# Performance work log

Measured on AMD Instinct MI355X. Metric: run time of the kernel, lower is better.

## Reference

```python
import jax, jax.numpy as jnp
import numpy as np

N_NODES = 50000
N_EDGES = 800000
IN_CH = 64
OUT_CH = 32
HEADS = 4
OUT_DIM = OUT_CH * HEADS  # concat=True -> 128
NEG_SLOPE = 0.2


def setup_inputs() -> dict:
    key = jax.random.key(0)
    ks = jax.random.split(key, 10)
    x = jax.random.normal(ks[0], (N_NODES, IN_CH), dtype=jnp.float32)
    edge_index = jax.random.randint(ks[1], (2, N_EDGES), 0, N_NODES, dtype=jnp.int64)
    s = 1.0 / np.sqrt(IN_CH)
    lin_w = jax.random.uniform(ks[2], (OUT_DIM, IN_CH), jnp.float32, -s, s)
    att_src = jax.random.uniform(ks[3], (HEADS, OUT_CH), jnp.float32, -s, s)
    att_dst = jax.random.uniform(ks[4], (HEADS, OUT_CH), jnp.float32, -s, s)
    gat_bias = jnp.zeros((OUT_DIM,), jnp.float32)
    res_w = jax.random.uniform(ks[5], (OUT_DIM, IN_CH), jnp.float32, -s, s)
    res_b = jax.random.uniform(ks[6], (OUT_DIM,), jnp.float32, -s, s)
    ln_g = jnp.ones((OUT_DIM,), jnp.float32)
    ln_b = jnp.zeros((OUT_DIM,), jnp.float32)
    return {"x": x, "edge_index": edge_index, "lin_w": lin_w, "att_src": att_src,
            "att_dst": att_dst, "gat_bias": gat_bias, "res_w": res_w, "res_b": res_b,
            "ln_g": ln_g, "ln_b": ln_b}


def reference(x, edge_index, lin_w, att_src, att_dst, gat_bias, res_w, res_b, ln_g, ln_b):
    N = x.shape[0]
    H, C = att_src.shape
    # PyG GATConv default: add self-loops
    loops = jnp.arange(N, dtype=edge_index.dtype)
    src = jnp.concatenate([edge_index[0], loops])  # [E+N]
    dst = jnp.concatenate([edge_index[1], loops])
    # linear transform -> [N, H, C]
    xt = (x @ lin_w.T).reshape(N, H, C)
    # per-node attention halves [N, H]
    a_src = (xt * att_src[None]).sum(-1)
    a_dst = (xt * att_dst[None]).sum(-1)
    # per-edge raw score with LeakyReLU(0.2) -> [E+N, H]
    e = jax.nn.leaky_relu(a_src[src] + a_dst[dst], NEG_SLOPE)
    # edge-softmax grouped by destination node (numerically stable)
    emax = jax.ops.segment_max(e, dst, num_segments=N)
    emax = jnp.where(jnp.isfinite(emax), emax, 0.0)
    ex = jnp.exp(e - emax[dst])
    esum = jax.ops.segment_sum(ex, dst, num_segments=N)
    alpha = ex / (esum[dst] + 1e-16)  # [E+N, H]
    # weighted message passing + scatter-add; concat heads
    msg = xt[src] * alpha[:, :, None]  # [E+N, H, C]
    h = jax.ops.segment_sum(msg, dst, num_segments=N).reshape(N, H * C) + gat_bias
    # residual linear + LayerNorm + LeakyReLU(0.2)
    z = h + x @ res_w.T + res_b
    mu = z.mean(-1, keepdims=True)
    var = ((z - mu) ** 2).mean(-1, keepdims=True)
    zn = (z - mu) * jax.lax.rsqrt(var + 1e-5) * ln_g + ln_b
    return jax.nn.leaky_relu(zn, NEG_SLOPE)
```

## Files before the change

### kernel.cpp

```cpp
#include <hip/hip_runtime.h>
#include <hip/hip_bf16.h>
#include <hip/hip_fp16.h>

typedef __hip_bfloat16 bf16;
typedef __attribute__((ext_vector_type(8))) short bf16x8;
typedef __attribute__((ext_vector_type(4))) float f32x4;

#define IN_CH   64
#define OUT_DIM 128
#define HEADS   4
#define NEG     0.2f
#define WPITCH  72
#define OPITCH  136
#define CAP     64
#define OVF_CAP 65536

__device__ __forceinline__ float lo_bf(unsigned int u) { return __uint_as_float(u << 16); }
__device__ __forceinline__ float hi_bf(unsigned int u) { return __uint_as_float(u & 0xffff0000u); }

__device__ __forceinline__ unsigned int pack_bf2(float a, float b) {
    unsigned int ua = (unsigned int)__bfloat16_as_ushort(__float2bfloat16(a));
    unsigned int ub = (unsigned int)__bfloat16_as_ushort(__float2bfloat16(b));
    return ua | (ub << 16);
}

__device__ __forceinline__ float ld(const void* p, size_t i, int isbf) {
    return isbf ? __bfloat162float(((const bf16*)p)[i]) : ((const float*)p)[i];
}

__device__ __forceinline__ int load_idx(const void* ei, int is64, long long pos) {
    if (is64) return (int)(((const long long*)ei)[pos]);
    return ((const int*)ei)[pos];
}

__global__ __launch_bounds__(256) void k0_init(const int* __restrict__ ei,
                                               const unsigned int* __restrict__ ln_g,
                                               int* __restrict__ flag,
                                               int* __restrict__ fill,
                                               int* __restrict__ ovf_cnt, int N) {
    int i = blockIdx.x * 256 + threadIdx.x;
    if (i < N) fill[i] = 0;
    if (i == 0) *ovf_cnt = 0;
    if (blockIdx.x == 0 && threadIdx.x < 64) {
        int lane = threadIdx.x;
        int v = ei[2 * lane + 1];
        unsigned long long b = __ballot(v != 0);
        if (lane == 0) {
            flag[0] = (b == 0ULL) ? 1 : 0;
            flag[1] = (ln_g[0] == 0x3F803F80u) ? 1 : 0;
        }
    }
}

__global__ __launch_bounds__(256, 3) void k1_transform(
    const void* __restrict__ x, const void* __restrict__ lin_w,
    const void* __restrict__ res_w, const void* __restrict__ att_src,
    const void* __restrict__ att_dst, const void* __restrict__ gat_bias,
    const void* __restrict__ res_b, const int* __restrict__ flag,
    const void* __restrict__ ei, int E,
    bf16* __restrict__ xt, bf16* __restrict__ resid,
    float* __restrict__ a_src, float* __restrict__ a_dst,
    int* __restrict__ fill, int* __restrict__ srcs_pad,
    unsigned long long* __restrict__ ovf, int* __restrict__ ovf_cnt, int N)
{
    __shared__ __align__(16) short wA[256 * WPITCH];
    __shared__ __align__(16) short xB[64 * WPITCH];
    int t = threadIdx.x;
    int isbf = flag[1];
    int is64 = flag[0];

    const long long stride = (long long)gridDim.x * 256;
    long long i0 = (long long)blockIdx.x * 256 + t;
    int es[4], ed[4]; bool ev[4];
    #pragma unroll
    for (int q = 0; q < 4; q++) {
        long long j = i0 + (long long)q * stride;
        ev[q] = (j < E);
        es[q] = 0; ed[q] = 0;
        if (ev[q]) {
            es[q] = load_idx(ei, is64, j);
            ed[q] = load_idx(ei, is64, (long long)E + j);
        }
    }

    {
        const void* src = (t < 128) ? lin_w : res_w;
        int row = (t < 128) ? t : (t - 128);
        short* dst = &wA[t * WPITCH];
        if (isbf) {
            const uint4* p = (const uint4*)((const bf16*)src + (size_t)row * 64);
            #pragma unroll
            for (int q = 0; q < 8; q++) ((uint4*)dst)[q] = p[q];
        } else {
            const float4* p = (const float4*)((const float*)src + (size_t)row * 64);
            #pragma unroll
            for (int q = 0; q < 16; q++) {
                float4 f = p[q];
                ((unsigned int*)dst)[2 * q]     = pack_bf2(f.x, f.y);
                ((unsigned int*)dst)[2 * q + 1] = pack_bf2(f.z, f.w);
            }
        }
    }

    {
        int j = t >> 2, part = t & 3;
        int gj = blockIdx.x * 64 + j;
        short* dst = &xB[j * WPITCH + part * 16];
        if (gj < N) {
            if (isbf) {
                const uint4* p = (const uint4*)((const bf16*)x + (size_t)gj * 64 + part * 16);
                ((uint4*)dst)[0] = p[0];
                ((uint4*)dst)[1] = p[1];
            } else {
                const float4* p = (const float4*)((const float*)x + (size_t)gj * 64 + part * 16);
                #pragma unroll
                for (int q = 0; q < 4; q++) {
                    float4 f = p[q];
                    ((unsigned int*)dst)[2 * q]     = pack_bf2(f.x, f.y);
                    ((unsigned int*)dst)[2 * q + 1] = pack_bf2(f.z, f.w);
                }
            }
        } else {
            ((uint4*)dst)[0] = make_uint4(0, 0, 0, 0);
            ((uint4*)dst)[1] = make_uint4(0, 0, 0, 0);
        }
    }
    __syncthreads();

    int w = t >> 6, lane = t & 63;
    int c = lane & 15, q = lane >> 4;

    bf16x8 afr[4][2];
    #pragma unroll
    for (int mt = 0; mt < 4; mt++) {
        #pragma unroll
        for (int kh = 0; kh < 2; kh++)
            afr[mt][kh] = *(const bf16x8*)&wA[(w * 64 + mt * 16 + c) * WPITCH + kh * 32 + q * 8];
    }

    int slot[4];
    #pragma unroll
    for (int q2 = 0; q2 < 4; q2++) {
        slot[q2] = 0;
        if (ev[q2]) {
            if ((unsigned)es[q2] >= (unsigned)N) es[q2] = 0;
            if ((unsigned)ed[q2] >= (unsigned)N) ed[q2] = 0;
            slot[q2] = atomicAdd(&fill[ed[q2]], 1);
        }
    }
    for (long long j = i0 + 4 * stride; j < E; j += stride) {
        int s = load_idx(ei, is64, j);
        int d = load_idx(ei, is64, (long long)E + j);
        if ((unsigned)s >= (unsigned)N) s = 0;
        if ((unsigned)d >= (unsigned)N) d = 0;
        int sl = atomicAdd(&fill[d], 1);
        if (sl < CAP) {
            srcs_pad[(size_t)d * CAP + sl] = s;
        } else {
            int k = atomicAdd(ovf_cnt, 1);
            if (k < OVF_CAP)
                ovf[k] = ((unsigned long long)(unsigned)d << 32) | (unsigned)s;
        }
    }

    f32x4 acc[4][4];
    #pragma unroll
    for (int mt = 0; mt < 4; mt++)
        #pragma unroll
        for (int nt = 0; nt < 4; nt++)
            acc[mt][nt] = (f32x4){0.f, 0.f, 0.f, 0.f};

    #pragma unroll
    for (int nt = 0; nt < 4; nt++) {
        bf16x8 b0 = *(const bf16x8*)&xB[(nt * 16 + c) * WPITCH + q * 8];
        bf16x8 b1 = *(const bf16x8*)&xB[(nt * 16 + c) * WPITCH + 32 + q * 8];
        #pragma unroll
        for (int mt = 0; mt < 4; mt++) {
            acc[mt][nt] = __builtin_amdgcn_mfma_f32_16x16x32_bf16(afr[mt][0], b0, acc[mt][nt], 0, 0, 0);
            acc[mt][nt] = __builtin_amdgcn_mfma_f32_16x16x32_bf16(afr[mt][1], b1, acc[mt][nt], 0, 0, 0);
        }
    }

    int isres = (w >= 2);
    int chw = (w & 1) * 64;

    float rb[4][4], atS[4][4], atD[4][4];
    #pragma unroll
    for (int mt = 0; mt < 4; mt++) {
        int ch0 = chw + mt * 16 + q * 4;
        #pragma unroll
        for (int r = 0; r < 4; r++) {
            if (isres) {
                rb[mt][r] = ld(res_b, ch0 + r, isbf) + ld(gat_bias, ch0 + r, isbf);
            } else {
                atS[mt][r] = ld(att_src, ch0 + r, isbf);
                atD[mt][r] = ld(att_dst, ch0 + r, isbf);
            }
        }
    }

    #pragma unroll
    for (int nt = 0; nt < 4; nt++) {
        int gnode = blockIdx.x * 64 + nt * 16 + c;
        float pS0 = 0.f, pS1 = 0.f, pD0 = 0.f, pD1 = 0.f;
        #pragma unroll
        for (int mt = 0; mt < 4; mt++) {
            if (isres) {
                acc[mt][nt][0] += rb[mt][0];
                acc[mt][nt][1] += rb[mt][1];
                acc[mt][nt][2] += rb[mt][2];
                acc[mt][nt][3] += rb[mt][3];
            } else {
                float v0 = acc[mt][nt][0], v1 = acc[mt][nt][1];
                float v2 = acc[mt][nt][2], v3 = acc[mt][nt][3];
                float s = v0 * atS[mt][0] + v1 * atS[mt][1] + v2 * atS[mt][2] + v3 * atS[mt][3];
                float d = v0 * atD[mt][0] + v1 * atD[mt][1] + v2 * atD[mt][2] + v3 * atD[mt][3];
                if (mt < 2) { pS0 += s; pD0 += d; } else { pS1 += s; pD1 += d; }
            }
        }
        if (!isres) {
            pS0 += __shfl_xor(pS0, 16, 64); pS0 += __shfl_xor(pS0, 32, 64);
            pS1 += __shfl_xor(pS1, 16, 64); pS1 += __shfl_xor(pS1, 32, 64);
            pD0 += __shfl_xor(pD0, 16, 64); pD0 += __shfl_xor(pD0, 32, 64);
            pD1 += __shfl_xor(pD1, 16, 64); pD1 += __shfl_xor(pD1, 32, 64);
            if (q == 0 && gnode < N) {
                int hb = (w & 1) * 2;
                *(float2*)&a_src[(size_t)gnode * HEADS + hb] = make_float2(pS0, pS1);
                *(float2*)&a_dst[(size_t)gnode * HEADS + hb] = make_float2(pD0, pD1);
            }
        }
    }

    __syncthreads();
    unsigned int* sOut = (unsigned int*)wA;
    #pragma unroll
    for (int nt = 0; nt < 4; nt++) {
        int node = nt * 16 + c;
        #pragma unroll
        for (int mt = 0; mt < 4; mt++) {
            int chc = w * 64 + mt * 16 + q * 4;
            uint2 uu = make_uint2(pack_bf2(acc[mt][nt][0], acc[mt][nt][1]),
                                  pack_bf2(acc[mt][nt][2], acc[mt][nt][3]));
            *(uint2*)&sOut[node * OPITCH + (chc >> 1)] = uu;
        }
    }
    __syncthreads();

    int tile0 = blockIdx.x * 64;
    int nvalid = N - tile0; if (nvalid > 64) nvalid = 64;
    unsigned int* xtw = (unsigned int*)xt;
    unsigned int* rsw = (unsigned int*)resid;
    #pragma unroll
    for (int i = 0; i < 4; i++) {
        int uidx = i * 1024 + t * 4;
        int node = uidx >> 6;
        int c2   = uidx & 63;
        if (node < nvalid) {
            uint4 vx = *(uint4*)&sOut[node * OPITCH + c2];
            *(uint4*)&xtw[(size_t)(tile0 + node) * 64 + c2] = vx;
            uint4 vr = *(uint4*)&sOut[node * OPITCH + 64 + c2];
            *(uint4*)&rsw[(size_t)(tile0 + node) * 64 + c2] = vr;
        }
    }

    #pragma unroll
    for (int q2 = 0; q2 < 4; q2++) {
        if (ev[q2]) {
            if (slot[q2] < CAP) {
                srcs_pad[(size_t)ed[q2] * CAP + slot[q2]] = es[q2];
            } else {
                int k = atomicAdd(ovf_cnt, 1);
                if (k < OVF_CAP)
                    ovf[k] = ((unsigned long long)(unsigned)ed[q2] << 32) | (unsigned)es[q2];
            }
        }
    }
}

__global__ __launch_bounds__(256) void k3_gather(
    const int* __restrict__ fill, const int* __restrict__ srcs_pad,
    const unsigned long long* __restrict__ ovf, const int* __restrict__ ovf_cnt,
    const unsigned int* __restrict__ xtu, const unsigned int* __restrict__ residu,
    const float* __restrict__ a_src, const float* __restrict__ a_dst,
    const void* __restrict__ ln_g, const void* __restrict__ ln_b,
    const int* __restrict__ flag, void* __restrict__ out, int N)
{
    int node = (int)((blockIdx.x * 256 + threadIdx.x) >> 6);
    int lane = threadIdx.x & 63;
    if (node >= N) return;
    int isbf = flag[1];
    int h = lane >> 4;

    float adh = a_dst[(size_t)node * HEADS + h];
    float ash = a_src[(size_t)node * HEADS + h];
    float e0 = ash + adh;
    e0 = e0 > 0.f ? e0 : e0 * NEG;
    float p = __expf(e0);
    unsigned int u = xtu[(size_t)node * 64 + lane];
    float acc0 = p * lo_bf(u);
    float acc1 = p * hi_bf(u);
    float esum = p;

    int deg = fill[node];
    int end = deg < CAP ? deg : CAP;
    const int* sp = srcs_pad + (size_t)node * CAP;
    int ee = 0;
    for (; ee + 8 <= end; ee += 8) {
        int s[8];
        #pragma unroll
        for (int q = 0; q < 8; q++) s[q] = sp[ee + q];
        float av[8];
        #pragma unroll
        for (int q = 0; q < 8; q++) av[q] = a_src[(size_t)s[q] * HEADS + h];
        unsigned int uv[8];
        #pragma unroll
        for (int q = 0; q < 8; q++) uv[q] = xtu[(size_t)s[q] * 64 + lane];
        #pragma unroll
        for (int q = 0; q < 8; q++) {
            float sc = av[q] + adh;
            sc = sc > 0.f ? sc : sc * NEG;
            float pe = __expf(sc);
            acc0 = fmaf(pe, lo_bf(uv[q]), acc0);
            acc1 = fmaf(pe, hi_bf(uv[q]), acc1);
            esum += pe;
        }
    }
    for (; ee < end; ++ee) {
        int s = sp[ee];
        float as = a_src[(size_t)s * HEADS + h];
        float sc = as + adh;
        sc = sc > 0.f ? sc : sc * NEG;
        float pe = __expf(sc);
        unsigned int us = xtu[(size_t)s * 64 + lane];
        acc0 = fmaf(pe, lo_bf(us), acc0);
        acc1 = fmaf(pe, hi_bf(us), acc1);
        esum += pe;
    }

    int oc = *ovf_cnt;
    if (oc > 0) {
        if (oc > OVF_CAP) oc = OVF_CAP;
        for (int k = 0; k < oc; k++) {
            unsigned long long pr = ovf[k];
            if ((int)(pr >> 32) == node) {
                int s = (int)(unsigned)pr;
                float as = a_src[(size_t)s * HEADS + h];
                float sc = as + adh;
                sc = sc > 0.f ? sc : sc * NEG;
                float pe = __expf(sc);
                unsigned int us = xtu[(size_t)s * 64 + lane];
                acc0 = fmaf(pe, lo_bf(us), acc0);
                acc1 = fmaf(pe, hi_bf(us), acc1);
                esum += pe;
            }
        }
    }

    float inv = 1.f / (esum + 1e-16f);
    unsigned int ur = residu[(size_t)node * 64 + lane];
    float z0 = fmaf(acc0, inv, lo_bf(ur));
    float z1 = fmaf(acc1, inv, hi_bf(ur));

    float s1 = z0 + z1;
    float s2 = z0 * z0 + z1 * z1;
    #pragma unroll
    for (int m = 1; m < 64; m <<= 1) {
        s1 += __shfl_xor(s1, m, 64);
        s2 += __shfl_xor(s2, m, 64);
    }
    float mu  = s1 * (1.0f / OUT_DIM);
    float var = s2 * (1.0f / OUT_DIM) - mu * mu;
    float rstd = rsqrtf(var + 1e-5f);
    int c0 = 2 * lane, c1 = 2 * lane + 1;
    float y0 = (z0 - mu) * rstd * ld(ln_g, c0, isbf) + ld(ln_b, c0, isbf);
    float y1 = (z1 - mu) * rstd * ld(ln_g, c1, isbf) + ld(ln_b, c1, isbf);
    y0 = y0 > 0.f ? y0 : y0 * NEG;
    y1 = y1 > 0.f ? y1 : y1 * NEG;
    if (isbf) {
        ((unsigned int*)out)[(size_t)node * 64 + lane] = pack_bf2(y0, y1);
    } else {
        ((float2*)out)[(size_t)node * 64 + lane] = make_float2(y0, y1);
    }
}

extern "C" void kernel_launch(void* const* d_in, const int* in_sizes, int n_in,
                              void* d_out, int out_size, void* d_ws, size_t ws_size,
                              hipStream_t stream)
{
    const void* x        = d_in[0];
    const void* ei       = d_in[1];
    const void* lin_w    = d_in[2];
    const void* att_src  = d_in[3];
    const void* att_dst  = d_in[4];
    const void* gat_bias = d_in[5];
    const void* res_w    = d_in[6];
    const void* res_b    = d_in[7];
    const void* ln_g     = d_in[8];
    const void* ln_b     = d_in[9];

    int N  = in_sizes[0] / IN_CH;
    int E  = in_sizes[1] / 2;

    int*   flag    = (int*)d_ws;
    int*   ovf_cnt = flag + 4;
    float* a_src   = (float*)(flag + 8);
    float* a_dst   = a_src + (size_t)N * HEADS;
    int*   fill    = (int*)(a_dst + (size_t)N * HEADS);
    unsigned long long* ovf =
        (unsigned long long*)(((uintptr_t)(fill + N) + 7) & ~(uintptr_t)7);
    int*   srcs_pad = (int*)(ovf + OVF_CAP);
    bf16*  xt      = (bf16*)(srcs_pad + (size_t)N * CAP);
    bf16*  resid   = xt + (size_t)N * OUT_DIM;

    int tiles = (N + 63) / 64;

    k0_init<<<(N + 255) / 256, 256, 0, stream>>>((const int*)ei,
                                                 (const unsigned int*)ln_g,
                                                 flag, fill, ovf_cnt, N);
    k1_transform<<<tiles, 256, 0, stream>>>(x, lin_w, res_w, att_src, att_dst,
                                            gat_bias, res_b, flag, ei, E,
                                            xt, resid, a_src, a_dst,
                                            fill, srcs_pad, ovf, ovf_cnt, N);
    k3_gather<<<(N + 3) / 4, 256, 0, stream>>>(fill, srcs_pad, ovf, ovf_cnt,
                                               (const unsigned int*)xt,
                                               (const unsigned int*)resid,
                                               a_src, a_dst, ln_g, ln_b, flag,
                                               d_out, N);
}
```

Before: 195.5 us.

## Load neighbor indices once per wave and broadcast via shuffles in gather

The gather kernel now has each lane load one entry of the node's padded source list up front and broadcast indices with wave shuffles. Previously every lane re-read the same indices from global memory. The loop is unrolled by 16 with masked tail contributions, which removes the scalar remainder loop and exposes more independent loads. The GEMM kernel's two __syncthreads are replaced by an inline-asm LDS-wait plus s_barrier. The masked tail wastes gather loads of node 0 for padded slots, and the 16-wide arrays raise register pressure.

```diff
diff --git a/kernel.cpp b/kernel.cpp
--- a/kernel.cpp
+++ b/kernel.cpp
@@ -31,6 +31,10 @@
 __device__ __forceinline__ int load_idx(const void* ei, int is64, long long pos) {
     if (is64) return (int)(((const long long*)ei)[pos]);
     return ((const int*)ei)[pos];
+}
+
+__device__ __forceinline__ void lds_barrier() {
+    asm volatile("s_waitcnt lgkmcnt(0)\n\ts_barrier" ::: "memory");
 }
 
 __global__ __launch_bounds__(256) void k0_init(const int* __restrict__ ei,
@@ -231,7 +235,7 @@
         }
     }
 
-    __syncthreads();
+    lds_barrier();
     unsigned int* sOut = (unsigned int*)wA;
     #pragma unroll
     for (int nt = 0; nt < 4; nt++) {
@@ -244,7 +248,7 @@
             *(uint2*)&sOut[node * OPITCH + (chc >> 1)] = uu;
         }
     }
-    __syncthreads();
+    lds_barrier();
 
     int tile0 = blockIdx.x * 64;
     int nvalid = N - tile0; if (nvalid > 64) nvalid = 64;
@@ -291,6 +295,10 @@
     int isbf = flag[1];
     int h = lane >> 4;
 
+    int deg = fill[node];
+    int end = deg < CAP ? deg : CAP;
+    int myS = (lane < end) ? srcs_pad[(size_t)node * CAP + lane] : 0;
+
     float adh = a_dst[(size_t)node * HEADS + h];
     float ash = a_src[(size_t)node * HEADS + h];
     float e0 = ash + adh;
@@ -301,40 +309,29 @@
     float acc1 = p * hi_bf(u);
     float esum = p;
 
-    int deg = fill[node];
-    int end = deg < CAP ? deg : CAP;
-    const int* sp = srcs_pad + (size_t)node * CAP;
-    int ee = 0;
-    for (; ee + 8 <= end; ee += 8) {
-        int s[8];
-        #pragma unroll
-        for (int q = 0; q < 8; q++) s[q] = sp[ee + q];
-        float av[8];
-        #pragma unroll
-        for (int q = 0; q < 8; q++) av[q] = a_src[(size_t)s[q] * HEADS + h];
-        unsigned int uv[8];
-        #pragma unroll
-        for (int q = 0; q < 8; q++) uv[q] = xtu[(size_t)s[q] * 64 + lane];
-        #pragma unroll
-        for (int q = 0; q < 8; q++) {
+    for (int ee = 0; ee < end; ee += 16) {
+        int   sarr[16];
+        float av[16];
+        unsigned int uv[16];
+        #pragma unroll
+        for (int q = 0; q < 16; q++)
+            sarr[q] = __shfl(myS, (ee + q) & 63, 64);
+        #pragma unroll
+        for (int q = 0; q < 16; q++)
+            av[q] = a_src[(size_t)sarr[q] * HEADS + h];
+        #pragma unroll
+        for (int q = 0; q < 16; q++)
+            uv[q] = xtu[(size_t)sarr[q] * 64 + lane];
+        #pragma unroll
+        for (int q = 0; q < 16; q++) {
             float sc = av[q] + adh;
             sc = sc > 0.f ? sc : sc * NEG;
             float pe = __expf(sc);
+            pe = (ee + q < end) ? pe : 0.f;
             acc0 = fmaf(pe, lo_bf(uv[q]), acc0);
             acc1 = fmaf(pe, hi_bf(uv[q]), acc1);
             esum += pe;
         }
-    }
-    for (; ee < end; ++ee) {
-        int s = sp[ee];
-        float as = a_src[(size_t)s * HEADS + h];
-        float sc = as + adh;
-        sc = sc > 0.f ? sc : sc * NEG;
-        float pe = __expf(sc);
-        unsigned int us = xtu[(size_t)s * 64 + lane];
-        acc0 = fmaf(pe, lo_bf(us), acc0);
-        acc1 = fmaf(pe, hi_bf(us), acc1);
-        esum += pe;
     }
 
     int oc = *ovf_cnt;
```

New measurement: 197.2 us. About the same (+0.9%).
